# Optimization experiments

Measured on AMD Instinct MI355X. Metric: run time of the kernel, lower is better.

## Reference

```python
import jax, jax.numpy as jnp
import numpy as np

B, F, R, O = 32768, 64, 64, 64  # batch, in_features, rules, out_features


def setup_inputs() -> dict:
    key = jax.random.key(0)
    k1, k2, k3, k4, k5 = jax.random.split(key, 5)
    X = jax.random.normal(k1, (B, F), dtype=jnp.float32)
    tt = jax.random.normal(k2, (1, F, R), dtype=jnp.float32) * 0.01
    mean = jax.random.normal(k3, (1, F, R), dtype=jnp.float32)
    # std is a learned positive scale (set by _rule_initialization); keep it away from 0
    std = jax.random.uniform(k4, (1, F, R), dtype=jnp.float32, minval=0.5, maxval=1.5)
    W = jax.random.normal(k5, (O, R * (F + 1)), dtype=jnp.float32) * 0.02  # nn.Linear weight [out, in]
    return {"X": X, "tt": tt, "mean": mean, "std": std, "W": W}


def reference(X, tt, mean, std, W):
    t = jnp.tanh(tt)                                  # [1,F,R]
    z = (X[:, :, None] - mean) / std                  # [B,F,R]
    g = jnp.exp(-(z * z))                             # Gaussian membership [B,F,R]
    m = g * t + 0.5 * (1.0 - t)                       # affine blend toward 0.5
    fire = jnp.prod(m, axis=1)                        # product t-norm over features -> [B,R]
    w = fire / jnp.sum(fire, axis=1, keepdims=True)   # normalize over rules
    ones = jnp.ones((X.shape[0], 1), dtype=X.dtype)
    Xa = jnp.concatenate([X, ones], axis=1)           # [B,F+1]
    feat = (Xa[:, :, None] * w[:, None, :]).reshape(X.shape[0], -1)  # [B,(F+1)*R], row-major (f outer, r inner)
    return feat @ W.T                                 # [B,O]
```

## Files before the change

### kernel.cpp

```cpp
#include <hip/hip_runtime.h>
#include <hip/hip_bf16.h>

#define F 64
#define R 64
#define O 64
#define BLOCK_B 64

typedef short bf16x8 __attribute__((ext_vector_type(8)));
typedef float f32x4 __attribute__((ext_vector_type(4)));
typedef float f32x2 __attribute__((ext_vector_type(2)));

static __device__ __forceinline__ short f2bf(float f) {
    unsigned u = __builtin_bit_cast(unsigned, f);
    unsigned r = (u + 0x7fffu + ((u >> 16) & 1u)) >> 16;
    return (short)r;
}

__global__ __launch_bounds__(256) void fq_prep(
        const float* __restrict__ tt, const float* __restrict__ mean,
        const float* __restrict__ std_, const float* __restrict__ W,
        float* __restrict__ prm, unsigned short* __restrict__ Wpk)
{
    const int blk = blockIdx.x;
    const int t   = threadIdx.x;
    if (blk < 65) {
        const int f = blk;
        __shared__ __align__(16) float ws[64][68];
#pragma unroll
        for (int i = 0; i < 16; ++i) {
            const int o = i * 4 + (t >> 6);
            const int r = t & 63;
            ws[o][r] = W[(size_t)o * 4160 + f * 64 + r];
        }
        __syncthreads();
#pragma unroll
        for (int half = 0; half < 2; ++half) {
            const int u8   = half * 256 + t;
            const int lane = u8 & 63;
            const int kk   = (u8 >> 6) & 1;
            const int nt   = u8 >> 7;
            const int o    = nt * 16 + (lane & 15);
            const int rb   = ((lane >> 4) << 3) + kk * 32;
            f32x4 a = *(const f32x4*)&ws[o][rb];
            f32x4 b = *(const f32x4*)&ws[o][rb + 4];
            unsigned short v[8];
            v[0] = (unsigned short)f2bf(a[0]); v[1] = (unsigned short)f2bf(a[1]);
            v[2] = (unsigned short)f2bf(a[2]); v[3] = (unsigned short)f2bf(a[3]);
            v[4] = (unsigned short)f2bf(b[0]); v[5] = (unsigned short)f2bf(b[1]);
            v[6] = (unsigned short)f2bf(b[2]); v[7] = (unsigned short)f2bf(b[3]);
            const int dst = ((nt * 65 + f) * 2 + kk) * 64 + lane;
            *(bf16x8*)(Wpk + (size_t)dst * 8) = *(bf16x8*)v;
        }
    } else {
#pragma unroll
        for (int i = 0; i < 16; ++i) {
            const int u = i * 256 + t;
            float sd = std_[u];
            float mn = mean[u];
            float th = tanhf(tt[u]);
            float s  = 1.2011224087864498f / sd;
            float4 p;
            p.x = s;
            p.y = mn * s;
            p.z = th;
            p.w = 0.5f * (1.0f - th);
            ((float4*)prm)[u] = p;
        }
    }
}

__global__ __launch_bounds__(256, 2) void fq_main(
        const float* __restrict__ X,
        const float4* __restrict__ prm,
        const bf16x8* __restrict__ Wp,
        float* __restrict__ out)
{
    __shared__ __align__(16) float xt[64][68];
    __shared__ __align__(16) float fire_lds[64][68];
    __shared__ float rinv[BLOCK_B];

    const int t    = threadIdx.x;
    const int lane = t & 63;
    const int w    = __builtin_amdgcn_readfirstlane(t >> 6);
    const int b0   = blockIdx.x * BLOCK_B;

    {
        const int f4 = (t & 15) * 4;
        const int r0 = t >> 4;
#pragma unroll
        for (int it = 0; it < 4; ++it) {
            const int row = r0 + 16 * it;
            float4 xv = *(const float4*)(X + (size_t)(b0 + row) * 64 + f4);
            xt[f4 + 0][row] = xv.x;
            xt[f4 + 1][row] = xv.y;
            xt[f4 + 2][row] = xv.z;
            xt[f4 + 3][row] = xv.w;
        }
    }

    {
        f32x2 fire2[8];
#pragma unroll
        for (int i = 0; i < 8; ++i) fire2[i] = (f32x2){1.f, 1.f};
        const float* Xw = X + (size_t)(b0 + 16 * w) * 64;
#pragma unroll 2
        for (int f = 0; f < F; ++f) {
            float4 p = prm[f * 64 + lane];
            f32x2 t2 = (f32x2){p.z, p.z};
            f32x2 c2 = (f32x2){p.w, p.w};
#pragma unroll
            for (int i = 0; i < 8; ++i) {
                float x0 = Xw[(2 * i) * 64 + f];
                float x1 = Xw[(2 * i + 1) * 64 + f];
                f32x2 z;
                z.x = __builtin_fmaf(x0, p.x, -p.y);
                z.y = __builtin_fmaf(x1, p.x, -p.y);
                f32x2 nz = -(z * z);
                f32x2 g;
                g.x = __builtin_amdgcn_exp2f(nz.x);
                g.y = __builtin_amdgcn_exp2f(nz.y);
                fire2[i] *= g * t2 + c2;
            }
        }
#pragma unroll
        for (int i = 0; i < 8; ++i) {
            fire_lds[16 * w + 2 * i][lane]     = fire2[i].x;
            fire_lds[16 * w + 2 * i + 1][lane] = fire2[i].y;
        }
    }
    __syncthreads();

    {
        const int row = t >> 2;
        const int c16 = (t & 3) * 16;
        f32x4 s0 = *(const f32x4*)&fire_lds[row][c16];
        f32x4 s1 = *(const f32x4*)&fire_lds[row][c16 + 4];
        f32x4 s2 = *(const f32x4*)&fire_lds[row][c16 + 8];
        f32x4 s3 = *(const f32x4*)&fire_lds[row][c16 + 12];
        float s = ((s0[0] + s0[1]) + (s0[2] + s0[3])) +
                  ((s1[0] + s1[1]) + (s1[2] + s1[3])) +
                  ((s2[0] + s2[1]) + (s2[2] + s2[3])) +
                  ((s3[0] + s3[1]) + (s3[2] + s3[3]));
        s += __shfl_xor(s, 1);
        s += __shfl_xor(s, 2);
        if ((t & 3) == 0) rinv[row] = 1.0f / s;
    }
    __syncthreads();

    const int m_in = lane & 15;
    const int quad = lane >> 4;
    const int nt   = w;
    const int q8   = quad * 8;

    bf16x8 wfrag[4][2];
#pragma unroll
    for (int m = 0; m < 4; ++m) {
        const int myrow = 16 * m + m_in;
        const float rs  = rinv[myrow];
#pragma unroll
        for (int kk = 0; kk < 2; ++kk) {
            f32x4 a = *(const f32x4*)&fire_lds[myrow][q8 + kk * 32];
            f32x4 b = *(const f32x4*)&fire_lds[myrow][q8 + kk * 32 + 4];
            wfrag[m][kk][0] = f2bf(a[0] * rs); wfrag[m][kk][1] = f2bf(a[1] * rs);
            wfrag[m][kk][2] = f2bf(a[2] * rs); wfrag[m][kk][3] = f2bf(a[3] * rs);
            wfrag[m][kk][4] = f2bf(b[0] * rs); wfrag[m][kk][5] = f2bf(b[1] * rs);
            wfrag[m][kk][6] = f2bf(b[2] * rs); wfrag[m][kk][7] = f2bf(b[3] * rs);
        }
    }

    const bf16x8* wpb = Wp + (size_t)(nt * 130) * 64 + lane;

    f32x4 acc[4];
#pragma unroll
    for (int m = 0; m < 4; ++m) acc[m] = (f32x4){0.f, 0.f, 0.f, 0.f};
    const f32x4 z4 = (f32x4){0.f, 0.f, 0.f, 0.f};

#pragma unroll 4
    for (int f = 0; f < F; ++f) {
        bf16x8 bb0 = wpb[(2 * f) * 64];
        bf16x8 bb1 = wpb[(2 * f + 1) * 64];
#pragma unroll
        for (int m = 0; m < 4; ++m) {
            f32x4 U = __builtin_amdgcn_mfma_f32_16x16x32_bf16(wfrag[m][0], bb0, z4, 0, 0, 0);
            U = __builtin_amdgcn_mfma_f32_16x16x32_bf16(wfrag[m][1], bb1, U, 0, 0, 0);
            f32x4 xv = *(const f32x4*)&xt[f][16 * m + quad * 4];
#pragma unroll
            for (int reg = 0; reg < 4; ++reg)
                acc[m][reg] = __builtin_fmaf(xv[reg], U[reg], acc[m][reg]);
        }
    }

    {
        bf16x8 bb0 = wpb[128 * 64];
        bf16x8 bb1 = wpb[129 * 64];
#pragma unroll
        for (int m = 0; m < 4; ++m) {
            f32x4 U = __builtin_amdgcn_mfma_f32_16x16x32_bf16(wfrag[m][0], bb0, z4, 0, 0, 0);
            U = __builtin_amdgcn_mfma_f32_16x16x32_bf16(wfrag[m][1], bb1, U, 0, 0, 0);
#pragma unroll
            for (int reg = 0; reg < 4; ++reg)
                acc[m][reg] += U[reg];
        }
    }

#pragma unroll
    for (int m = 0; m < 4; ++m)
#pragma unroll
        for (int reg = 0; reg < 4; ++reg) {
            const int row = b0 + 16 * m + quad * 4 + reg;
            out[(size_t)row * 64 + nt * 16 + m_in] = acc[m][reg];
        }
}

extern "C" void kernel_launch(void* const* d_in, const int* in_sizes, int n_in,
                              void* d_out, int out_size, void* d_ws, size_t ws_size,
                              hipStream_t stream) {
    const float* X    = (const float*)d_in[0];
    const float* tt   = (const float*)d_in[1];
    const float* mean = (const float*)d_in[2];
    const float* std_ = (const float*)d_in[3];
    const float* W    = (const float*)d_in[4];
    float* out = (float*)d_out;

    float* prm = (float*)d_ws;
    unsigned short* Wpk = (unsigned short*)((char*)d_ws + 65536);

    fq_prep<<<66, 256, 0, stream>>>(tt, mean, std_, W, prm, Wpk);

    const int nblocks = 32768 / BLOCK_B;
    fq_main<<<nblocks, 256, 0, stream>>>(X, (const float4*)prm,
                                         (const bf16x8*)Wpk, out);
}
```

Measured before the change: 117.4 us.

## Double threads per block, split GEMM K across wave pairs, read X from LDS

The main kernel now runs 512 threads. Eight waves each compute membership products for 8 rows. The input tile is read from the transposed LDS copy instead of strided global loads, and rule parameters are prefetched one feature ahead. The GEMM stage splits the feature loop between two waves per output tile, software-prefetches the next packed weight fragments, and reduces the two partial accumulators through an added LDS buffer before the store. The prep kernel is flattened to one element group per thread across more blocks, which removes its LDS staging. The extra LDS and sync raise per-block resource use and may limit the number of resident blocks.

```diff
diff --git a/kernel.cpp b/kernel.cpp
--- a/kernel.cpp
+++ b/kernel.cpp
@@ -21,55 +21,37 @@
         const float* __restrict__ std_, const float* __restrict__ W,
         float* __restrict__ prm, unsigned short* __restrict__ Wpk)
 {
-    const int blk = blockIdx.x;
-    const int t   = threadIdx.x;
-    if (blk < 65) {
-        const int f = blk;
-        __shared__ __align__(16) float ws[64][68];
-#pragma unroll
-        for (int i = 0; i < 16; ++i) {
-            const int o = i * 4 + (t >> 6);
-            const int r = t & 63;
-            ws[o][r] = W[(size_t)o * 4160 + f * 64 + r];
-        }
-        __syncthreads();
-#pragma unroll
-        for (int half = 0; half < 2; ++half) {
-            const int u8   = half * 256 + t;
-            const int lane = u8 & 63;
-            const int kk   = (u8 >> 6) & 1;
-            const int nt   = u8 >> 7;
-            const int o    = nt * 16 + (lane & 15);
-            const int rb   = ((lane >> 4) << 3) + kk * 32;
-            f32x4 a = *(const f32x4*)&ws[o][rb];
-            f32x4 b = *(const f32x4*)&ws[o][rb + 4];
-            unsigned short v[8];
-            v[0] = (unsigned short)f2bf(a[0]); v[1] = (unsigned short)f2bf(a[1]);
-            v[2] = (unsigned short)f2bf(a[2]); v[3] = (unsigned short)f2bf(a[3]);
-            v[4] = (unsigned short)f2bf(b[0]); v[5] = (unsigned short)f2bf(b[1]);
-            v[6] = (unsigned short)f2bf(b[2]); v[7] = (unsigned short)f2bf(b[3]);
-            const int dst = ((nt * 65 + f) * 2 + kk) * 64 + lane;
-            *(bf16x8*)(Wpk + (size_t)dst * 8) = *(bf16x8*)v;
-        }
-    } else {
-#pragma unroll
-        for (int i = 0; i < 16; ++i) {
-            const int u = i * 256 + t;
-            float sd = std_[u];
-            float mn = mean[u];
-            float th = tanhf(tt[u]);
-            float s  = 1.2011224087864498f / sd;
-            float4 p;
-            p.x = s;
-            p.y = mn * s;
-            p.z = th;
-            p.w = 0.5f * (1.0f - th);
-            ((float4*)prm)[u] = p;
-        }
-    }
-}
-
-__global__ __launch_bounds__(256, 2) void fq_main(
+    const int tg = blockIdx.x * 256 + threadIdx.x;
+    if (tg < 65 * 512) {
+        const int f    = tg >> 9;
+        const int u8   = tg & 511;
+        const int lane = u8 & 63;
+        const int kk   = (u8 >> 6) & 1;
+        const int nt   = u8 >> 7;
+        const int o    = nt * 16 + (lane & 15);
+        const int rb   = ((lane >> 4) << 3) + kk * 32;
+        const float* src = W + o * 4160 + f * 64 + rb;
+        unsigned short v[8];
+#pragma unroll
+        for (int j = 0; j < 8; ++j) v[j] = (unsigned short)f2bf(src[j]);
+        const int dst = ((nt * 65 + f) * 2 + kk) * 64 + lane;
+        *(bf16x8*)(Wpk + (size_t)dst * 8) = *(bf16x8*)v;
+    } else if (tg < 65 * 512 + 4096) {
+        const int u = tg - 65 * 512;
+        float sd = std_[u];
+        float mn = mean[u];
+        float th = tanhf(tt[u]);
+        float s  = 1.2011224087864498f / sd;
+        float4 p;
+        p.x = s;
+        p.y = mn * s;
+        p.z = th;
+        p.w = 0.5f * (1.0f - th);
+        ((float4*)prm)[u] = p;
+    }
+}
+
+__global__ __launch_bounds__(512, 4) void fq_main(
         const float* __restrict__ X,
         const float4* __restrict__ prm,
         const bf16x8* __restrict__ Wp,
@@ -78,6 +60,7 @@
     __shared__ __align__(16) float xt[64][68];
     __shared__ __align__(16) float fire_lds[64][68];
     __shared__ float rinv[BLOCK_B];
+    __shared__ __align__(16) float epi[4][4][64][4];
 
     const int t    = threadIdx.x;
     const int lane = t & 63;
@@ -88,8 +71,8 @@
         const int f4 = (t & 15) * 4;
         const int r0 = t >> 4;
 #pragma unroll
-        for (int it = 0; it < 4; ++it) {
-            const int row = r0 + 16 * it;
+        for (int it = 0; it < 2; ++it) {
+            const int row = r0 + 32 * it;
             float4 xv = *(const float4*)(X + (size_t)(b0 + row) * 64 + f4);
             xt[f4 + 0][row] = xv.x;
             xt[f4 + 1][row] = xv.y;
@@ -97,59 +80,69 @@
             xt[f4 + 3][row] = xv.w;
         }
     }
+    __syncthreads();
 
     {
-        f32x2 fire2[8];
-#pragma unroll
-        for (int i = 0; i < 8; ++i) fire2[i] = (f32x2){1.f, 1.f};
-        const float* Xw = X + (size_t)(b0 + 16 * w) * 64;
+        f32x2 fire2[4];
+#pragma unroll
+        for (int i = 0; i < 4; ++i) fire2[i] = (f32x2){1.f, 1.f};
+        const int r0 = 8 * w;
+        float4 p = prm[lane];
 #pragma unroll 2
         for (int f = 0; f < F; ++f) {
-            float4 p = prm[f * 64 + lane];
+            float4 pn = prm[(f + 1) * 64 + lane];
+            f32x4 xa = *(const f32x4*)&xt[f][r0];
+            f32x4 xb = *(const f32x4*)&xt[f][r0 + 4];
             f32x2 t2 = (f32x2){p.z, p.z};
             f32x2 c2 = (f32x2){p.w, p.w};
-#pragma unroll
-            for (int i = 0; i < 8; ++i) {
-                float x0 = Xw[(2 * i) * 64 + f];
-                float x1 = Xw[(2 * i + 1) * 64 + f];
-                f32x2 z;
-                z.x = __builtin_fmaf(x0, p.x, -p.y);
-                z.y = __builtin_fmaf(x1, p.x, -p.y);
-                f32x2 nz = -(z * z);
-                f32x2 g;
-                g.x = __builtin_amdgcn_exp2f(nz.x);
-                g.y = __builtin_amdgcn_exp2f(nz.y);
-                fire2[i] *= g * t2 + c2;
-            }
-        }
-#pragma unroll
-        for (int i = 0; i < 8; ++i) {
-            fire_lds[16 * w + 2 * i][lane]     = fire2[i].x;
-            fire_lds[16 * w + 2 * i + 1][lane] = fire2[i].y;
+            f32x2 z0, z1, z2, z3;
+            z0.x = __builtin_fmaf(xa[0], p.x, -p.y);
+            z0.y = __builtin_fmaf(xa[1], p.x, -p.y);
+            z1.x = __builtin_fmaf(xa[2], p.x, -p.y);
+            z1.y = __builtin_fmaf(xa[3], p.x, -p.y);
+            z2.x = __builtin_fmaf(xb[0], p.x, -p.y);
+            z2.y = __builtin_fmaf(xb[1], p.x, -p.y);
+            z3.x = __builtin_fmaf(xb[2], p.x, -p.y);
+            z3.y = __builtin_fmaf(xb[3], p.x, -p.y);
+            f32x2 n0 = -(z0 * z0), n1 = -(z1 * z1);
+            f32x2 n2 = -(z2 * z2), n3 = -(z3 * z3);
+            f32x2 g0, g1, g2, g3;
+            g0.x = __builtin_amdgcn_exp2f(n0.x); g0.y = __builtin_amdgcn_exp2f(n0.y);
+            g1.x = __builtin_amdgcn_exp2f(n1.x); g1.y = __builtin_amdgcn_exp2f(n1.y);
+            g2.x = __builtin_amdgcn_exp2f(n2.x); g2.y = __builtin_amdgcn_exp2f(n2.y);
+            g3.x = __builtin_amdgcn_exp2f(n3.x); g3.y = __builtin_amdgcn_exp2f(n3.y);
+            fire2[0] *= g0 * t2 + c2;
+            fire2[1] *= g1 * t2 + c2;
+            fire2[2] *= g2 * t2 + c2;
+            fire2[3] *= g3 * t2 + c2;
+            p = pn;
+        }
+#pragma unroll
+        for (int i = 0; i < 4; ++i) {
+            fire_lds[r0 + 2 * i][lane]     = fire2[i].x;
+            fire_lds[r0 + 2 * i + 1][lane] = fire2[i].y;
         }
     }
     __syncthreads();
 
     {
-        const int row = t >> 2;
-        const int c16 = (t & 3) * 16;
-        f32x4 s0 = *(const f32x4*)&fire_lds[row][c16];
-        f32x4 s1 = *(const f32x4*)&fire_lds[row][c16 + 4];
-        f32x4 s2 = *(const f32x4*)&fire_lds[row][c16 + 8];
-        f32x4 s3 = *(const f32x4*)&fire_lds[row][c16 + 12];
-        float s = ((s0[0] + s0[1]) + (s0[2] + s0[3])) +
-                  ((s1[0] + s1[1]) + (s1[2] + s1[3])) +
-                  ((s2[0] + s2[1]) + (s2[2] + s2[3])) +
-                  ((s3[0] + s3[1]) + (s3[2] + s3[3]));
+        const int row = t >> 3;
+        const int c8  = (t & 7) * 8;
+        f32x4 s0 = *(const f32x4*)&fire_lds[row][c8];
+        f32x4 s1 = *(const f32x4*)&fire_lds[row][c8 + 4];
+        float s = (s0[0] + s0[1]) + (s0[2] + s0[3]) +
+                  (s1[0] + s1[1]) + (s1[2] + s1[3]);
         s += __shfl_xor(s, 1);
         s += __shfl_xor(s, 2);
-        if ((t & 3) == 0) rinv[row] = 1.0f / s;
+        s += __shfl_xor(s, 4);
+        if ((t & 7) == 0) rinv[row] = 1.0f / s;
     }
     __syncthreads();
 
     const int m_in = lane & 15;
     const int quad = lane >> 4;
-    const int nt   = w;
+    const int nt   = w >> 1;
+    const int fh   = w & 1;
     const int q8   = quad * 8;
 
     bf16x8 wfrag[4][2];
@@ -169,16 +162,22 @@
     }
 
     const bf16x8* wpb = Wp + (size_t)(nt * 130) * 64 + lane;
+    const int s0 = fh * 32;
+    const int ns = 32;
 
     f32x4 acc[4];
 #pragma unroll
     for (int m = 0; m < 4; ++m) acc[m] = (f32x4){0.f, 0.f, 0.f, 0.f};
     const f32x4 z4 = (f32x4){0.f, 0.f, 0.f, 0.f};
 
-#pragma unroll 4
-    for (int f = 0; f < F; ++f) {
-        bf16x8 bb0 = wpb[(2 * f) * 64];
-        bf16x8 bb1 = wpb[(2 * f + 1) * 64];
+    bf16x8 nb0 = wpb[(2 * s0) * 64];
+    bf16x8 nb1 = wpb[(2 * s0 + 1) * 64];
+    for (int i = 0; i < ns; ++i) {
+        const int f  = s0 + i;
+        bf16x8 bb0 = nb0, bb1 = nb1;
+        const int sp = (f + 1 < 64) ? f + 1 : 64;
+        nb0 = wpb[(2 * sp) * 64];
+        nb1 = wpb[(2 * sp + 1) * 64];
 #pragma unroll
         for (int m = 0; m < 4; ++m) {
             f32x4 U = __builtin_amdgcn_mfma_f32_16x16x32_bf16(wfrag[m][0], bb0, z4, 0, 0, 0);
@@ -190,26 +189,32 @@
         }
     }
 
-    {
-        bf16x8 bb0 = wpb[128 * 64];
-        bf16x8 bb1 = wpb[129 * 64];
+    if (fh == 1) {
 #pragma unroll
         for (int m = 0; m < 4; ++m) {
-            f32x4 U = __builtin_amdgcn_mfma_f32_16x16x32_bf16(wfrag[m][0], bb0, z4, 0, 0, 0);
-            U = __builtin_amdgcn_mfma_f32_16x16x32_bf16(wfrag[m][1], bb1, U, 0, 0, 0);
+            f32x4 U = __builtin_amdgcn_mfma_f32_16x16x32_bf16(wfrag[m][0], nb0, z4, 0, 0, 0);
+            U = __builtin_amdgcn_mfma_f32_16x16x32_bf16(wfrag[m][1], nb1, U, 0, 0, 0);
 #pragma unroll
             for (int reg = 0; reg < 4; ++reg)
                 acc[m][reg] += U[reg];
         }
-    }
-
-#pragma unroll
-    for (int m = 0; m < 4; ++m)
-#pragma unroll
-        for (int reg = 0; reg < 4; ++reg) {
-            const int row = b0 + 16 * m + quad * 4 + reg;
-            out[(size_t)row * 64 + nt * 16 + m_in] = acc[m][reg];
-        }
+#pragma unroll
+        for (int m = 0; m < 4; ++m)
+            *(f32x4*)&epi[nt][m][lane][0] = acc[m];
+    }
+    __syncthreads();
+
+    if (fh == 0) {
+#pragma unroll
+        for (int m = 0; m < 4; ++m) {
+            f32x4 r = acc[m] + *(const f32x4*)&epi[nt][m][lane][0];
+#pragma unroll
+            for (int reg = 0; reg < 4; ++reg) {
+                const int row = b0 + 16 * m + quad * 4 + reg;
+                out[(size_t)row * 64 + nt * 16 + m_in] = r[reg];
+            }
+        }
+    }
 }
 
 extern "C" void kernel_launch(void* const* d_in, const int* in_sizes, int n_in,
@@ -225,9 +230,9 @@
     float* prm = (float*)d_ws;
     unsigned short* Wpk = (unsigned short*)((char*)d_ws + 65536);
 
-    fq_prep<<<66, 256, 0, stream>>>(tt, mean, std_, W, prm, Wpk);
+    fq_prep<<<146, 256, 0, stream>>>(tt, mean, std_, W, prm, Wpk);
 
     const int nblocks = 32768 / BLOCK_B;
-    fq_main<<<nblocks, 256, 0, stream>>>(X, (const float4*)prm,
+    fq_main<<<nblocks, 512, 0, stream>>>(X, (const float4*)prm,
                                          (const bf16x8*)Wpk, out);
 }
```

Measured after the change: 276.5 us. 136% more time.
